# Optimization experiments

Hardware: AMD Instinct MI355X
Metric: run time of the kernel (lower is better)

Reference implementation:

```python
import jax, jax.numpy as jnp
import numpy as np

PATCH = 4      # patch_size
WIN = 8        # win_size (== win_stride, non-overlapping windows)
TAU = 0.05     # sinkhorn_tau
ITERS = 20     # sinkhorn_iters
EPS = 1e-6


def setup_inputs() -> dict:
    key = jax.random.key(0)
    k0, k1 = jax.random.split(key)
    B, C, H, W = 16, 4, 256, 256
    z0 = jax.random.normal(k0, (B, C, H, W), jnp.float32)
    z1 = jax.random.normal(k1, (B, C, H, W), jnp.float32)
    return {"z0": z0, "z1": z1}


def _token_feats(z):
    # patchify_latents + L2 normalize (F.normalize eps clamp). groupmean proj
    # is identity since d_match == token_dim.
    B, C, H, W = z.shape
    hp, wp = H // PATCH, W // PATCH
    t = z.reshape(B, C, hp, PATCH, wp, PATCH).transpose(0, 2, 4, 1, 3, 5)
    t = t.reshape(B, hp, wp, C * PATCH * PATCH)          # (B,hp,wp,D)
    n = jnp.maximum(jnp.sqrt(jnp.sum(t * t, axis=-1, keepdims=True)), EPS)
    return t / n


def _to_windows(f):
    B, hp, wp, D = f.shape
    nh, nw = hp // WIN, wp // WIN
    w = f.reshape(B, nh, WIN, nw, WIN, D).transpose(0, 1, 3, 2, 4, 5)
    return w.reshape(B * nh * nw, WIN * WIN, D)


def _sinkhorn_log(logits):
    # _sinkhorn_log_batch: alternate row (dim 2) / col (dim 1) logsumexp
    def step(lp, _):
        lp = lp - jax.nn.logsumexp(lp, axis=2, keepdims=True)
        lp = lp - jax.nn.logsumexp(lp, axis=1, keepdims=True)
        return lp, None
    lp, _ = jax.lax.scan(step, logits, None, length=ITERS)
    return lp


def _grid_sample_border(img, gx, gy):
    # F.grid_sample bilinear, padding_mode='border', align_corners=True,
    # with gx/gy already in absolute pixel coords (B,H,W).
    B, C, H, W = img.shape
    gx = jnp.clip(gx, 0.0, W - 1.0)
    gy = jnp.clip(gy, 0.0, H - 1.0)
    x0f = jnp.floor(gx); y0f = jnp.floor(gy)
    wx = (gx - x0f)[:, None]; wy = (gy - y0f)[:, None]   # (B,1,H,W)
    x0 = jnp.clip(x0f.astype(jnp.int32), 0, W - 1)
    x1 = jnp.clip(x0 + 1, 0, W - 1)
    y0 = jnp.clip(y0f.astype(jnp.int32), 0, H - 1)
    y1 = jnp.clip(y0 + 1, 0, H - 1)
    flat = img.reshape(B, C, H * W)

    def gat(yi, xi):
        idx = (yi * W + xi).reshape(B, 1, H * W)
        idx = jnp.broadcast_to(idx, (B, C, H * W))
        return jnp.take_along_axis(flat, idx, axis=2).reshape(B, C, H, W)

    v00 = gat(y0, x0); v01 = gat(y0, x1)
    v10 = gat(y1, x0); v11 = gat(y1, x1)
    return (v00 * (1 - wx) * (1 - wy) + v01 * wx * (1 - wy)
            + v10 * (1 - wx) * wy + v11 * wx * wy)


def reference(z0, z1):
    B, C, H, W = z0.shape
    hp, wp = H // PATCH, W // PATCH
    nh, nw = hp // WIN, wp // WIN
    f0 = _token_feats(z0)
    f1 = _token_feats(z1)
    w0 = _to_windows(f0)                                  # (BW, M, D)
    w1 = _to_windows(f1)
    logits = jnp.einsum('wid,wjd->wij', w0, w1) / TAU     # (BW, M, M)
    logp = _sinkhorn_log(logits)
    Pm = jax.nn.softmax(logp, axis=-1)                    # row-normalized plan
    # expected target position per source token (local window coords, x/y)
    ys, xs = jnp.meshgrid(jnp.arange(WIN), jnp.arange(WIN), indexing='ij')
    pos = jnp.stack([xs.ravel(), ys.ravel()], axis=-1).astype(z0.dtype)  # (M,2)
    disp = Pm @ pos - pos                                 # (BW, M, 2) token units
    disp = disp.reshape(B, nh, nw, WIN, WIN, 2).transpose(0, 1, 3, 2, 4, 5)
    disp = disp.reshape(B, hp, wp, 2)
    # token flow -> pixel flow (nearest upsample, scale by patch size)
    flow = jnp.repeat(jnp.repeat(disp, PATCH, axis=1), PATCH, axis=2) * PATCH
    yy, xx = jnp.meshgrid(jnp.arange(H, dtype=z0.dtype),
                          jnp.arange(W, dtype=z0.dtype), indexing='ij')
    gx = xx[None] + flow[..., 0]
    gy = yy[None] + flow[..., 1]
    return _grid_sample_border(z1, gx, gy)
```

## Files before the change

kernel.cpp:

```cpp
#include <hip/hip_runtime.h>
#include <math.h>


#define S0 68

__global__ __launch_bounds__(256, 4)
void skw_kernel(const float* __restrict__ z0, const float* __restrict__ z1,
                float* __restrict__ out) {
    __shared__ float f0[64 * S0];
    __shared__ float f1t[64 * S0];
    __shared__ float psq[256];
    __shared__ float invn0[64], invn1[64];
    __shared__ float redbuf[256];
    __shared__ float rowr[64], colr[64];
    __shared__ float dispx[64], dispy[64];

    const int t  = threadIdx.x;
    const int blk = blockIdx.x;
    const int b  = blk >> 6;
    const int wy = (blk >> 3) & 7;
    const int wx = blk & 7;
    const int Y0 = wy * 32, X0 = wx * 32;

    const int xq = t & 7;
    const int yy = (t >> 3) & 31;
    const int mm = (yy >> 2) * 8 + xq;
    const int pi = yy & 3;

    {
        float a = 0.f;
        const float* src = z0 + (size_t)(b * 4) * 65536 + (size_t)(Y0 + yy) * 256 + X0 + xq * 4;
        #pragma unroll
        for (int c = 0; c < 4; ++c) {
            float4 v = *(const float4*)(src + c * 65536);
            a += v.x*v.x + v.y*v.y + v.z*v.z + v.w*v.w;
            *(float4*)&f0[mm * S0 + c * 16 + pi * 4] = v;
        }
        psq[t] = a;
    }
    __syncthreads();
    if (t < 64) {
        const int ti = t >> 3, tj = t & 7;
        float s = psq[(ti*4+0)*8+tj] + psq[(ti*4+1)*8+tj]
                + psq[(ti*4+2)*8+tj] + psq[(ti*4+3)*8+tj];
        invn0[t] = 1.0f / fmaxf(sqrtf(s), 1e-6f);
    }
    __syncthreads();
    {
        float a = 0.f;
        const float* src = z1 + (size_t)(b * 4) * 65536 + (size_t)(Y0 + yy) * 256 + X0 + xq * 4;
        #pragma unroll
        for (int c = 0; c < 4; ++c) {
            float4 v = *(const float4*)(src + c * 65536);
            a += v.x*v.x + v.y*v.y + v.z*v.z + v.w*v.w;
            const int d = c * 16 + pi * 4;
            f1t[(d+0)*S0 + mm] = v.x;
            f1t[(d+1)*S0 + mm] = v.y;
            f1t[(d+2)*S0 + mm] = v.z;
            f1t[(d+3)*S0 + mm] = v.w;
        }
        psq[t] = a;
    }
    __syncthreads();
    if (t < 64) {
        const int ti = t >> 3, tj = t & 7;
        float s = psq[(ti*4+0)*8+tj] + psq[(ti*4+1)*8+tj]
                + psq[(ti*4+2)*8+tj] + psq[(ti*4+3)*8+tj];
        invn1[t] = 1.0f / fmaxf(sqrtf(s), 1e-6f);
    }
    __syncthreads();

    const int bi = t >> 4, bj = t & 15;
    float acc[4][4];
    #pragma unroll
    for (int r = 0; r < 4; ++r)
        #pragma unroll
        for (int s2 = 0; s2 < 4; ++s2) acc[r][s2] = 0.f;

    #pragma unroll 4
    for (int dc = 0; dc < 16; ++dc) {
        float4 A[4], Bv[4];
        #pragma unroll
        for (int r = 0; r < 4; ++r) A[r] = *(const float4*)&f0[(bi*4+r)*S0 + dc*4];
        #pragma unroll
        for (int dd = 0; dd < 4; ++dd) Bv[dd] = *(const float4*)&f1t[(dc*4+dd)*S0 + bj*4];
        #pragma unroll
        for (int r = 0; r < 4; ++r) {
            acc[r][0] += A[r].x*Bv[0].x + A[r].y*Bv[1].x + A[r].z*Bv[2].x + A[r].w*Bv[3].x;
            acc[r][1] += A[r].x*Bv[0].y + A[r].y*Bv[1].y + A[r].z*Bv[2].y + A[r].w*Bv[3].y;
            acc[r][2] += A[r].x*Bv[0].z + A[r].y*Bv[1].z + A[r].z*Bv[2].z + A[r].w*Bv[3].z;
            acc[r][3] += A[r].x*Bv[0].w + A[r].y*Bv[1].w + A[r].z*Bv[2].w + A[r].w*Bv[3].w;
        }
    }
    float si[4], sj[4];
    #pragma unroll
    for (int r = 0; r < 4; ++r) si[r] = invn0[bi*4+r] * 20.0f;
    #pragma unroll
    for (int s2 = 0; s2 < 4; ++s2) sj[s2] = invn1[bj*4+s2];
    __syncthreads();
    float* Mm = f0;
    #pragma unroll
    for (int r = 0; r < 4; ++r) {
        float4 o;
        o.x = acc[r][0]*si[r]*sj[0];
        o.y = acc[r][1]*si[r]*sj[1];
        o.z = acc[r][2]*si[r]*sj[2];
        o.w = acc[r][3]*si[r]*sj[3];
        *(float4*)&Mm[(bi*4+r)*S0 + bj*4] = o;
    }
    __syncthreads();

    const int ri = t >> 2, q = t & 3;
    const int cbase = q * 16;

    {
        float v[16];
        #pragma unroll
        for (int u = 0; u < 4; ++u) {
            float4 x = *(const float4*)&Mm[ri*S0 + cbase + u*4];
            v[u*4+0]=x.x; v[u*4+1]=x.y; v[u*4+2]=x.z; v[u*4+3]=x.w;
        }
        float mx = v[0];
        #pragma unroll
        for (int k = 1; k < 16; ++k) mx = fmaxf(mx, v[k]);
        mx = fmaxf(mx, __shfl_xor(mx, 1));
        mx = fmaxf(mx, __shfl_xor(mx, 2));
        float s = 0.f;
        #pragma unroll
        for (int k = 0; k < 16; ++k) { v[k] = __expf(v[k] - mx); s += v[k]; }
        s += __shfl_xor(s, 1);
        s += __shfl_xor(s, 2);
        #pragma unroll
        for (int u = 0; u < 4; ++u)
            *(float4*)&Mm[ri*S0 + cbase + u*4] =
                make_float4(v[u*4+0], v[u*4+1], v[u*4+2], v[u*4+3]);
        if (q == 0) rowr[ri] = 1.0f / s;
    }
    __syncthreads();

    for (int it = 0; it < 20; ++it) {
        {
            const int j = t & 63, g = t >> 6;
            float part = 0.f;
            #pragma unroll
            for (int k = 0; k < 16; ++k) {
                const int i = g * 16 + k;
                float v = Mm[i*S0 + j] * rowr[i];
                Mm[i*S0 + j] = v;
                part += v;
            }
            redbuf[g*64 + j] = part;
        }
        __syncthreads();
        if (t < 64)
            colr[t] = 1.0f / (redbuf[t] + redbuf[64+t] + redbuf[128+t] + redbuf[192+t]);
        __syncthreads();
        if (it < 19) {
            float v[16], s = 0.f;
            #pragma unroll
            for (int u = 0; u < 4; ++u) {
                float4 x = *(const float4*)&Mm[ri*S0 + cbase + u*4];
                float4 c = *(const float4*)&colr[cbase + u*4];
                x.x *= c.x; x.y *= c.y; x.z *= c.z; x.w *= c.w;
                v[u*4+0]=x.x; v[u*4+1]=x.y; v[u*4+2]=x.z; v[u*4+3]=x.w;
                s += x.x + x.y + x.z + x.w;
            }
            s += __shfl_xor(s, 1);
            s += __shfl_xor(s, 2);
            #pragma unroll
            for (int u = 0; u < 4; ++u)
                *(float4*)&Mm[ri*S0 + cbase + u*4] =
                    make_float4(v[u*4+0], v[u*4+1], v[u*4+2], v[u*4+3]);
            if (q == 0) rowr[ri] = 1.0f / s;
            __syncthreads();
        }
    }

    {
        float s = 0.f, sx = 0.f, sy = 0.f;
        #pragma unroll
        for (int u = 0; u < 4; ++u) {
            float4 x = *(const float4*)&Mm[ri*S0 + cbase + u*4];
            float4 c = *(const float4*)&colr[cbase + u*4];
            float vv[4] = {x.x*c.x, x.y*c.y, x.z*c.z, x.w*c.w};
            #pragma unroll
            for (int k = 0; k < 4; ++k) {
                const int j = cbase + u*4 + k;
                s  += vv[k];
                sx += vv[k] * (float)(j & 7);
                sy += vv[k] * (float)(j >> 3);
            }
        }
        s  += __shfl_xor(s, 1);  s  += __shfl_xor(s, 2);
        sx += __shfl_xor(sx, 1); sx += __shfl_xor(sx, 2);
        sy += __shfl_xor(sy, 1); sy += __shfl_xor(sy, 2);
        if (q == 0) {
            const float inv = 1.0f / s;
            dispx[ri] = sx * inv - (float)(ri & 7);
            dispy[ri] = sy * inv - (float)(ri >> 3);
        }
    }
    __syncthreads();

    #pragma unroll
    for (int rep = 0; rep < 4; ++rep) {
        const int p = rep * 256 + t;
        const int y = p >> 5, x = p & 31;
        const int m2 = (y >> 2) * 8 + (x >> 2);
        float gx = (float)(X0 + x) + 4.0f * dispx[m2];
        float gy = (float)(Y0 + y) + 4.0f * dispy[m2];
        gx = fminf(fmaxf(gx, 0.0f), 255.0f);
        gy = fminf(fmaxf(gy, 0.0f), 255.0f);
        const float x0f = floorf(gx), y0f = floorf(gy);
        const float wxf = gx - x0f, wyf = gy - y0f;
        int xi0 = (int)x0f, yi0 = (int)y0f;
        const int xi1 = min(xi0 + 1, 255), yi1 = min(yi0 + 1, 255);
        const float w00 = (1.f-wxf)*(1.f-wyf), w01 = wxf*(1.f-wyf);
        const float w10 = (1.f-wxf)*wyf,       w11 = wxf*wyf;
        const float* basep = z1 + (size_t)(b * 4) * 65536;
        #pragma unroll
        for (int c = 0; c < 4; ++c) {
            const float* pc = basep + c * 65536;
            const float v00 = pc[yi0*256 + xi0], v01 = pc[yi0*256 + xi1];
            const float v10 = pc[yi1*256 + xi0], v11 = pc[yi1*256 + xi1];
            out[((size_t)(b*4+c)*256 + (Y0+y))*256 + X0 + x]
                = v00*w00 + v01*w01 + v10*w10 + v11*w11;
        }
    }
}

extern "C" void kernel_launch(void* const* d_in, const int* in_sizes, int n_in,
                              void* d_out, int out_size, void* d_ws, size_t ws_size,
                              hipStream_t stream) {
    (void)in_sizes; (void)n_in; (void)d_ws; (void)ws_size; (void)out_size;
    const float* z0 = (const float*)d_in[0];
    const float* z1 = (const float*)d_in[1];
    float* out = (float*)d_out;
    skw_kernel<<<dim3(1024), dim3(256), 0, stream>>>(z0, z1, out);
}
```

Before: 122.8 us.

## Run Sinkhorn as scaling vectors in registers, one wave per window

Each block now processes four windows. It computes all four 64x64 similarity matrices into shared memory, then gives each wavefront one window. The wave holds exp(K) and its transpose in registers and iterates Sinkhorn in the u/v scaling-vector form, broadcasting with readlane. This removes the per-iteration shared-memory read/modify/write passes and the block-wide barriers of the old log-domain-equivalent loop. The trade-offs are 128 registers per thread for K/KT, fewer blocks (256 instead of 1024), and dropping the max-subtraction before exp. That works only because the logits are bounded by 1/tau = 20.

```diff
diff --git a/kernel.cpp b/kernel.cpp
--- a/kernel.cpp
+++ b/kernel.cpp
@@ -4,216 +4,197 @@
 
 #define S0 68
 
-__global__ __launch_bounds__(256, 4)
+__device__ __forceinline__ float rlane(float v, int l) {
+    return __uint_as_float(__builtin_amdgcn_readlane(__float_as_uint(v), l));
+}
+
+__global__ __launch_bounds__(256, 1)
 void skw_kernel(const float* __restrict__ z0, const float* __restrict__ z1,
                 float* __restrict__ out) {
-    __shared__ float f0[64 * S0];
+    __shared__ float f0 [64 * S0];
     __shared__ float f1t[64 * S0];
-    __shared__ float psq[256];
+    __shared__ float Mw [4 * 64 * S0];
+    __shared__ float psq0[256], psq1[256];
     __shared__ float invn0[64], invn1[64];
-    __shared__ float redbuf[256];
-    __shared__ float rowr[64], colr[64];
-    __shared__ float dispx[64], dispy[64];
-
-    const int t  = threadIdx.x;
+    __shared__ float dispxA[256], dispyA[256];
+
+    const int t   = threadIdx.x;
     const int blk = blockIdx.x;
-    const int b  = blk >> 6;
-    const int wy = (blk >> 3) & 7;
-    const int wx = blk & 7;
-    const int Y0 = wy * 32, X0 = wx * 32;
+    const int b   = blk >> 4;
+    const int wy  = (blk >> 1) & 7;
+    const int wxq = blk & 1;
+    const int Y0  = wy * 32;
+    const int XB  = wxq * 128;
 
     const int xq = t & 7;
     const int yy = (t >> 3) & 31;
     const int mm = (yy >> 2) * 8 + xq;
     const int pi = yy & 3;
 
+    const int wv   = t >> 6;
+    const int lane = t & 63;
+
+    #pragma unroll 1
+    for (int w = 0; w < 4; ++w) {
+        const int X0 = XB + w * 32;
+        {
+            const size_t base = (size_t)(b * 4) * 65536 + (size_t)(Y0 + yy) * 256 + X0 + xq * 4;
+            const float* s0p = z0 + base;
+            const float* s1p = z1 + base;
+            float a0 = 0.f;
+            #pragma unroll
+            for (int c = 0; c < 4; ++c) {
+                float4 vv = *(const float4*)(s0p + c * 65536);
+                a0 += vv.x*vv.x + vv.y*vv.y + vv.z*vv.z + vv.w*vv.w;
+                *(float4*)&f0[mm * S0 + c * 16 + pi * 4] = vv;
+            }
+            psq0[t] = a0;
+            float a1 = 0.f;
+            #pragma unroll
+            for (int c = 0; c < 4; ++c) {
+                float4 vv = *(const float4*)(s1p + c * 65536);
+                a1 += vv.x*vv.x + vv.y*vv.y + vv.z*vv.z + vv.w*vv.w;
+                const int d = c * 16 + pi * 4;
+                f1t[(d+0)*S0 + mm] = vv.x;
+                f1t[(d+1)*S0 + mm] = vv.y;
+                f1t[(d+2)*S0 + mm] = vv.z;
+                f1t[(d+3)*S0 + mm] = vv.w;
+            }
+            psq1[t] = a1;
+        }
+        __syncthreads();
+        if (t < 128) {
+            const int u2 = t & 63;
+            const float* ps = (t < 64) ? psq0 : psq1;
+            const int ti = u2 >> 3, tj = u2 & 7;
+            float s = ps[(ti*4+0)*8+tj] + ps[(ti*4+1)*8+tj]
+                    + ps[(ti*4+2)*8+tj] + ps[(ti*4+3)*8+tj];
+            float r = 1.0f / fmaxf(sqrtf(s), 1e-6f);
+            if (t < 64) invn0[u2] = r; else invn1[u2] = r;
+        }
+        __syncthreads();
+
+        const int bi = t >> 4, bj = t & 15;
+        float acc[4][4];
+        #pragma unroll
+        for (int r = 0; r < 4; ++r)
+            #pragma unroll
+            for (int s2 = 0; s2 < 4; ++s2) acc[r][s2] = 0.f;
+
+        #pragma unroll 4
+        for (int dc = 0; dc < 16; ++dc) {
+            float4 A[4], Bv[4];
+            #pragma unroll
+            for (int r = 0; r < 4; ++r) A[r] = *(const float4*)&f0[(bi*4+r)*S0 + dc*4];
+            #pragma unroll
+            for (int dd = 0; dd < 4; ++dd) Bv[dd] = *(const float4*)&f1t[(dc*4+dd)*S0 + bj*4];
+            #pragma unroll
+            for (int r = 0; r < 4; ++r) {
+                acc[r][0] += A[r].x*Bv[0].x + A[r].y*Bv[1].x + A[r].z*Bv[2].x + A[r].w*Bv[3].x;
+                acc[r][1] += A[r].x*Bv[0].y + A[r].y*Bv[1].y + A[r].z*Bv[2].y + A[r].w*Bv[3].y;
+                acc[r][2] += A[r].x*Bv[0].z + A[r].y*Bv[1].z + A[r].z*Bv[2].z + A[r].w*Bv[3].z;
+                acc[r][3] += A[r].x*Bv[0].w + A[r].y*Bv[1].w + A[r].z*Bv[2].w + A[r].w*Bv[3].w;
+            }
+        }
+        float si[4], sj[4];
+        #pragma unroll
+        for (int r = 0; r < 4; ++r)  si[r] = invn0[bi*4+r] * 20.0f;
+        #pragma unroll
+        for (int s2 = 0; s2 < 4; ++s2) sj[s2] = invn1[bj*4+s2];
+        float* Mo = &Mw[w * (64 * S0)];
+        #pragma unroll
+        for (int r = 0; r < 4; ++r) {
+            float4 o;
+            o.x = acc[r][0]*si[r]*sj[0];
+            o.y = acc[r][1]*si[r]*sj[1];
+            o.z = acc[r][2]*si[r]*sj[2];
+            o.w = acc[r][3]*si[r]*sj[3];
+            *(float4*)&Mo[(bi*4+r)*S0 + bj*4] = o;
+        }
+        __syncthreads();
+    }
+
+    const float* Mb = &Mw[wv * (64 * S0)];
+    float K[64], KT[64];
+    #pragma unroll
+    for (int j4 = 0; j4 < 16; ++j4) {
+        float4 r4 = *(const float4*)&Mb[lane * S0 + j4 * 4];
+        K[4*j4+0] = __expf(r4.x); K[4*j4+1] = __expf(r4.y);
+        K[4*j4+2] = __expf(r4.z); K[4*j4+3] = __expf(r4.w);
+    }
+    #pragma unroll
+    for (int j = 0; j < 64; ++j) KT[j] = __expf(Mb[j * S0 + lane]);
+
+    float u, v;
     {
-        float a = 0.f;
-        const float* src = z0 + (size_t)(b * 4) * 65536 + (size_t)(Y0 + yy) * 256 + X0 + xq * 4;
-        #pragma unroll
-        for (int c = 0; c < 4; ++c) {
-            float4 v = *(const float4*)(src + c * 65536);
-            a += v.x*v.x + v.y*v.y + v.z*v.z + v.w*v.w;
-            *(float4*)&f0[mm * S0 + c * 16 + pi * 4] = v;
-        }
-        psq[t] = a;
+        float s0=0.f, s1=0.f, s2=0.f, s3=0.f;
+        #pragma unroll
+        for (int j = 0; j < 64; j += 4) {
+            s0 += K[j]; s1 += K[j+1]; s2 += K[j+2]; s3 += K[j+3];
+        }
+        u = 1.0f / ((s0+s1) + (s2+s3));
+    }
+    #pragma unroll 1
+    for (int it = 0; it < 19; ++it) {
+        float s0=0.f, s1=0.f, s2=0.f, s3=0.f;
+        #pragma unroll
+        for (int j = 0; j < 64; j += 4) {
+            s0 = fmaf(KT[j  ], rlane(u, j  ), s0);
+            s1 = fmaf(KT[j+1], rlane(u, j+1), s1);
+            s2 = fmaf(KT[j+2], rlane(u, j+2), s2);
+            s3 = fmaf(KT[j+3], rlane(u, j+3), s3);
+        }
+        v = 1.0f / ((s0+s1) + (s2+s3));
+        s0=0.f; s1=0.f; s2=0.f; s3=0.f;
+        #pragma unroll
+        for (int j = 0; j < 64; j += 4) {
+            s0 = fmaf(K[j  ], rlane(v, j  ), s0);
+            s1 = fmaf(K[j+1], rlane(v, j+1), s1);
+            s2 = fmaf(K[j+2], rlane(v, j+2), s2);
+            s3 = fmaf(K[j+3], rlane(v, j+3), s3);
+        }
+        u = 1.0f / ((s0+s1) + (s2+s3));
+    }
+    {
+        float s0=0.f, s1=0.f, s2=0.f, s3=0.f;
+        #pragma unroll
+        for (int j = 0; j < 64; j += 4) {
+            s0 = fmaf(KT[j  ], rlane(u, j  ), s0);
+            s1 = fmaf(KT[j+1], rlane(u, j+1), s1);
+            s2 = fmaf(KT[j+2], rlane(u, j+2), s2);
+            s3 = fmaf(KT[j+3], rlane(u, j+3), s3);
+        }
+        v = 1.0f / ((s0+s1) + (s2+s3));
+    }
+    {
+        float ss=0.f, sx=0.f, sy=0.f;
+        #pragma unroll
+        for (int j = 0; j < 64; ++j) {
+            float pj = K[j] * rlane(v, j);
+            ss += pj;
+            sx = fmaf(pj, (float)(j & 7),  sx);
+            sy = fmaf(pj, (float)(j >> 3), sy);
+        }
+        const float inv = 1.0f / ss;
+        dispxA[t] = sx * inv - (float)(lane & 7);
+        dispyA[t] = sy * inv - (float)(lane >> 3);
     }
     __syncthreads();
-    if (t < 64) {
-        const int ti = t >> 3, tj = t & 7;
-        float s = psq[(ti*4+0)*8+tj] + psq[(ti*4+1)*8+tj]
-                + psq[(ti*4+2)*8+tj] + psq[(ti*4+3)*8+tj];
-        invn0[t] = 1.0f / fmaxf(sqrtf(s), 1e-6f);
-    }
-    __syncthreads();
-    {
-        float a = 0.f;
-        const float* src = z1 + (size_t)(b * 4) * 65536 + (size_t)(Y0 + yy) * 256 + X0 + xq * 4;
-        #pragma unroll
-        for (int c = 0; c < 4; ++c) {
-            float4 v = *(const float4*)(src + c * 65536);
-            a += v.x*v.x + v.y*v.y + v.z*v.z + v.w*v.w;
-            const int d = c * 16 + pi * 4;
-            f1t[(d+0)*S0 + mm] = v.x;
-            f1t[(d+1)*S0 + mm] = v.y;
-            f1t[(d+2)*S0 + mm] = v.z;
-            f1t[(d+3)*S0 + mm] = v.w;
-        }
-        psq[t] = a;
-    }
-    __syncthreads();
-    if (t < 64) {
-        const int ti = t >> 3, tj = t & 7;
-        float s = psq[(ti*4+0)*8+tj] + psq[(ti*4+1)*8+tj]
-                + psq[(ti*4+2)*8+tj] + psq[(ti*4+3)*8+tj];
-        invn1[t] = 1.0f / fmaxf(sqrtf(s), 1e-6f);
-    }
-    __syncthreads();
-
-    const int bi = t >> 4, bj = t & 15;
-    float acc[4][4];
-    #pragma unroll
-    for (int r = 0; r < 4; ++r)
-        #pragma unroll
-        for (int s2 = 0; s2 < 4; ++s2) acc[r][s2] = 0.f;
-
-    #pragma unroll 4
-    for (int dc = 0; dc < 16; ++dc) {
-        float4 A[4], Bv[4];
-        #pragma unroll
-        for (int r = 0; r < 4; ++r) A[r] = *(const float4*)&f0[(bi*4+r)*S0 + dc*4];
-        #pragma unroll
-        for (int dd = 0; dd < 4; ++dd) Bv[dd] = *(const float4*)&f1t[(dc*4+dd)*S0 + bj*4];
-        #pragma unroll
-        for (int r = 0; r < 4; ++r) {
-            acc[r][0] += A[r].x*Bv[0].x + A[r].y*Bv[1].x + A[r].z*Bv[2].x + A[r].w*Bv[3].x;
-            acc[r][1] += A[r].x*Bv[0].y + A[r].y*Bv[1].y + A[r].z*Bv[2].y + A[r].w*Bv[3].y;
-            acc[r][2] += A[r].x*Bv[0].z + A[r].y*Bv[1].z + A[r].z*Bv[2].z + A[r].w*Bv[3].z;
-            acc[r][3] += A[r].x*Bv[0].w + A[r].y*Bv[1].w + A[r].z*Bv[2].w + A[r].w*Bv[3].w;
-        }
-    }
-    float si[4], sj[4];
-    #pragma unroll
-    for (int r = 0; r < 4; ++r) si[r] = invn0[bi*4+r] * 20.0f;
-    #pragma unroll
-    for (int s2 = 0; s2 < 4; ++s2) sj[s2] = invn1[bj*4+s2];
-    __syncthreads();
-    float* Mm = f0;
-    #pragma unroll
-    for (int r = 0; r < 4; ++r) {
-        float4 o;
-        o.x = acc[r][0]*si[r]*sj[0];
-        o.y = acc[r][1]*si[r]*sj[1];
-        o.z = acc[r][2]*si[r]*sj[2];
-        o.w = acc[r][3]*si[r]*sj[3];
-        *(float4*)&Mm[(bi*4+r)*S0 + bj*4] = o;
-    }
-    __syncthreads();
-
-    const int ri = t >> 2, q = t & 3;
-    const int cbase = q * 16;
-
-    {
-        float v[16];
-        #pragma unroll
-        for (int u = 0; u < 4; ++u) {
-            float4 x = *(const float4*)&Mm[ri*S0 + cbase + u*4];
-            v[u*4+0]=x.x; v[u*4+1]=x.y; v[u*4+2]=x.z; v[u*4+3]=x.w;
-        }
-        float mx = v[0];
-        #pragma unroll
-        for (int k = 1; k < 16; ++k) mx = fmaxf(mx, v[k]);
-        mx = fmaxf(mx, __shfl_xor(mx, 1));
-        mx = fmaxf(mx, __shfl_xor(mx, 2));
-        float s = 0.f;
-        #pragma unroll
-        for (int k = 0; k < 16; ++k) { v[k] = __expf(v[k] - mx); s += v[k]; }
-        s += __shfl_xor(s, 1);
-        s += __shfl_xor(s, 2);
-        #pragma unroll
-        for (int u = 0; u < 4; ++u)
-            *(float4*)&Mm[ri*S0 + cbase + u*4] =
-                make_float4(v[u*4+0], v[u*4+1], v[u*4+2], v[u*4+3]);
-        if (q == 0) rowr[ri] = 1.0f / s;
-    }
-    __syncthreads();
-
-    for (int it = 0; it < 20; ++it) {
-        {
-            const int j = t & 63, g = t >> 6;
-            float part = 0.f;
-            #pragma unroll
-            for (int k = 0; k < 16; ++k) {
-                const int i = g * 16 + k;
-                float v = Mm[i*S0 + j] * rowr[i];
-                Mm[i*S0 + j] = v;
-                part += v;
-            }
-            redbuf[g*64 + j] = part;
-        }
-        __syncthreads();
-        if (t < 64)
-            colr[t] = 1.0f / (redbuf[t] + redbuf[64+t] + redbuf[128+t] + redbuf[192+t]);
-        __syncthreads();
-        if (it < 19) {
-            float v[16], s = 0.f;
-            #pragma unroll
-            for (int u = 0; u < 4; ++u) {
-                float4 x = *(const float4*)&Mm[ri*S0 + cbase + u*4];
-                float4 c = *(const float4*)&colr[cbase + u*4];
-                x.x *= c.x; x.y *= c.y; x.z *= c.z; x.w *= c.w;
-                v[u*4+0]=x.x; v[u*4+1]=x.y; v[u*4+2]=x.z; v[u*4+3]=x.w;
-                s += x.x + x.y + x.z + x.w;
-            }
-            s += __shfl_xor(s, 1);
-            s += __shfl_xor(s, 2);
-            #pragma unroll
-            for (int u = 0; u < 4; ++u)
-                *(float4*)&Mm[ri*S0 + cbase + u*4] =
-                    make_float4(v[u*4+0], v[u*4+1], v[u*4+2], v[u*4+3]);
-            if (q == 0) rowr[ri] = 1.0f / s;
-            __syncthreads();
-        }
-    }
-
-    {
-        float s = 0.f, sx = 0.f, sy = 0.f;
-        #pragma unroll
-        for (int u = 0; u < 4; ++u) {
-            float4 x = *(const float4*)&Mm[ri*S0 + cbase + u*4];
-            float4 c = *(const float4*)&colr[cbase + u*4];
-            float vv[4] = {x.x*c.x, x.y*c.y, x.z*c.z, x.w*c.w};
-            #pragma unroll
-            for (int k = 0; k < 4; ++k) {
-                const int j = cbase + u*4 + k;
-                s  += vv[k];
-                sx += vv[k] * (float)(j & 7);
-                sy += vv[k] * (float)(j >> 3);
-            }
-        }
-        s  += __shfl_xor(s, 1);  s  += __shfl_xor(s, 2);
-        sx += __shfl_xor(sx, 1); sx += __shfl_xor(sx, 2);
-        sy += __shfl_xor(sy, 1); sy += __shfl_xor(sy, 2);
-        if (q == 0) {
-            const float inv = 1.0f / s;
-            dispx[ri] = sx * inv - (float)(ri & 7);
-            dispy[ri] = sy * inv - (float)(ri >> 3);
-        }
-    }
-    __syncthreads();
-
-    #pragma unroll
-    for (int rep = 0; rep < 4; ++rep) {
+
+    #pragma unroll 2
+    for (int rep = 0; rep < 16; ++rep) {
         const int p = rep * 256 + t;
-        const int y = p >> 5, x = p & 31;
-        const int m2 = (y >> 2) * 8 + (x >> 2);
-        float gx = (float)(X0 + x) + 4.0f * dispx[m2];
-        float gy = (float)(Y0 + y) + 4.0f * dispy[m2];
+        const int y = p >> 7;
+        const int x = p & 127;
+        const int m2 = ((y >> 2) << 3) + ((x & 31) >> 2);
+        const int widx = (x >> 5) * 64 + m2;
+        float gx = (float)(XB + x) + 4.0f * dispxA[widx];
+        float gy = (float)(Y0 + y) + 4.0f * dispyA[widx];
         gx = fminf(fmaxf(gx, 0.0f), 255.0f);
         gy = fminf(fmaxf(gy, 0.0f), 255.0f);
         const float x0f = floorf(gx), y0f = floorf(gy);
         const float wxf = gx - x0f, wyf = gy - y0f;
-        int xi0 = (int)x0f, yi0 = (int)y0f;
+        const int xi0 = (int)x0f, yi0 = (int)y0f;
         const int xi1 = min(xi0 + 1, 255), yi1 = min(yi0 + 1, 255);
         const float w00 = (1.f-wxf)*(1.f-wyf), w01 = wxf*(1.f-wyf);
         const float w10 = (1.f-wxf)*wyf,       w11 = wxf*wyf;
@@ -223,7 +204,7 @@
             const float* pc = basep + c * 65536;
             const float v00 = pc[yi0*256 + xi0], v01 = pc[yi0*256 + xi1];
             const float v10 = pc[yi1*256 + xi0], v11 = pc[yi1*256 + xi1];
-            out[((size_t)(b*4+c)*256 + (Y0+y))*256 + X0 + x]
+            out[((size_t)(b*4+c)*256 + (Y0+y))*256 + XB + x]
                 = v00*w00 + v01*w01 + v10*w10 + v11*w11;
         }
     }
@@ -236,5 +217,5 @@
     const float* z0 = (const float*)d_in[0];
     const float* z1 = (const float*)d_in[1];
     float* out = (float*)d_out;
-    skw_kernel<<<dim3(1024), dim3(256), 0, stream>>>(z0, z1, out);
+    skw_kernel<<<dim3(256), dim3(256), 0, stream>>>(z0, z1, out);
 }
```

Result: faster. 108.0 us (-12.1%).
